# Kernel tuning notes

Hardware: AMD Instinct MI355X
Metric: run time of the kernel (lower is better)

The kernel has to match this reference:

```python
import jax, jax.numpy as jnp
import numpy as np

B, C, H, W = 32, 128, 56, 56
O = 256
KH, KW = 3, 3
SH, SW = 1, 1
PH, PW = 1, 1
T = 6          # num_terms
R = 8          # low_rank
D = C * KH * KW          # 1152
R2 = R * KH * KW         # 72


def setup_inputs() -> dict:
    key = jax.random.key(0)
    ks = jax.random.split(key, 6)
    scale = 0.05
    return {
        "x": jax.random.normal(ks[0], (B, C, H, W), dtype=jnp.float32),
        "S1s": jax.random.normal(ks[1], (T, D, R), dtype=jnp.float32) * scale,
        "U1s": jax.random.normal(ks[2], (T, R, O), dtype=jnp.float32) * scale,
        "U2s": jax.random.normal(ks[3], (T, R2, D), dtype=jnp.float32) * scale,
        "S2s": jax.random.normal(ks[4], (T, R2, O), dtype=jnp.float32) * scale,
        "bias": jax.random.normal(ks[5], (O,), dtype=jnp.float32) * scale,
    }


def _extract_windows(x):
    # im2col: pad then gather strided windows; d flattened in (C, kh, kw) order
    xp = jnp.pad(x, ((0, 0), (0, 0), (PH, PH), (PW, PW)))
    Hp, Wp = xp.shape[2], xp.shape[3]
    Ho = (Hp - KH) // SH + 1
    Wo = (Wp - KW) // SW + 1
    # stack KH*KW shifted views -> [B, C, KH*KW, Ho, Wo]
    patches = jnp.stack(
        [xp[:, :, i:i + SH * Ho:SH, j:j + SW * Wo:SW]
         for i in range(KH) for j in range(KW)],
        axis=2,
    )
    # -> [B, Ho, Wo, C, KH*KW] -> [N, C*KH*KW]
    xw = patches.transpose(0, 3, 4, 1, 2).reshape(B * Ho * Wo, D)
    return xw, Ho, Wo


def reference(x, S1s, U1s, U2s, S2s, bias):
    xw, Ho, Wo = _extract_windows(x)                    # [N, D]
    # term 1: x_windows @ S1s[t] @ U1s[t], averaged over terms
    out1 = jnp.einsum('nd,tdr,tro->no', xw, S1s, U1s, optimize=True) / T + bias
    # term 2: x_windows @ U2s[t].T @ S2s[t], averaged over terms
    out2 = jnp.einsum('nd,tdr,tro->no', xw, jnp.swapaxes(U2s, 1, 2), S2s,
                      optimize=True) / T
    # NOTE: bias is added twice, faithfully matching the original module
    out = (out1 + out2 + bias).reshape(B, Ho, Wo, O).transpose(0, 3, 1, 2)
    return out
```

## Files before the change

kernel.cpp:

```cpp
#include <hip/hip_runtime.h>
#include <hip/hip_bf16.h>

typedef __attribute__((ext_vector_type(8))) short  short8;
typedef __attribute__((ext_vector_type(8))) unsigned short ushort8;
typedef __attribute__((ext_vector_type(4))) unsigned short usv4;
typedef __attribute__((ext_vector_type(4))) float  f32x4;

#define D_DIM 1152
#define O_DIM 256
#define N_TOT 100352
#define XT_H 58
#define XT_ROW (58 * 128)

__device__ __forceinline__ unsigned short f2bf(float f) {
  __hip_bfloat16 h = __float2bfloat16(f);
  return __builtin_bit_cast(unsigned short, h);
}

#define GLOAD_LDS16(g, l)                                              \
  __builtin_amdgcn_global_load_lds(                                    \
      (const __attribute__((address_space(1))) void*)(g),              \
      (__attribute__((address_space(3))) void*)(l), 16, 0, 0)

__global__ __launch_bounds__(256) void wt_kernel(
    const float* __restrict__ S1s, const float* __restrict__ U1s,
    const float* __restrict__ U2s, const float* __restrict__ S2s,
    unsigned short* __restrict__ Wt) {
  __shared__ float A_lds[32][64];
  __shared__ float B_lds[32][64];

  const int bo = blockIdx.x & 3;
  const int bd = blockIdx.x >> 2;
  const int o0  = bo << 6;
  const int dn0 = bd << 6;
  const int rr  = dn0 >> 7;
  const int c0  = dn0 & 127;

  const int tid = threadIdx.x;
  const int ty = tid >> 4, tx = tid & 15;

  float acc[4][4] = {};

  for (int kc = 0; kc < 15; ++kc) {
#pragma unroll
    for (int e = 0; e < 8; ++e) {
      const int li = e * 256 + tid;
      const int kk = li >> 6;
      const int xx = li & 63;
      const int k  = kc * 32 + kk;
      float av, bv;
      if (k < 48) {
        av = U1s[k * O_DIM + o0 + xx];
        const int d_old = (c0 + xx) * 9 + rr;
        bv = S1s[(size_t)((k >> 3) * D_DIM + d_old) * 8 + (k & 7)];
      } else {
        const int kq = k - 48;
        av = S2s[(size_t)kq * O_DIM + o0 + xx];
        const int d_old = (c0 + xx) * 9 + rr;
        bv = U2s[(size_t)kq * D_DIM + d_old];
      }
      A_lds[kk][xx] = av;
      B_lds[kk][xx] = bv;
    }
    __syncthreads();
#pragma unroll
    for (int kk = 0; kk < 32; ++kk) {
      f32x4 a = *(const f32x4*)&A_lds[kk][ty << 2];
      f32x4 b = *(const f32x4*)&B_lds[kk][tx << 2];
#pragma unroll
      for (int i = 0; i < 4; ++i)
#pragma unroll
        for (int j = 0; j < 4; ++j)
          acc[i][j] += a[i] * b[j];
    }
    __syncthreads();
  }

#pragma unroll
  for (int i = 0; i < 4; ++i) {
    usv4 v;
#pragma unroll
    for (int j = 0; j < 4; ++j) v[j] = f2bf(acc[i][j] * (1.0f / 6.0f));
    *(usv4*)(Wt + (size_t)(o0 + (ty << 2) + i) * D_DIM + dn0 + (tx << 2)) = v;
  }
}

__global__ __launch_bounds__(256) void pad_kernel(const float* __restrict__ x,
                                                  unsigned short* __restrict__ xt) {
  int blk = blockIdx.x;
  int b = blk / XT_H, ih = blk - b * XT_H;
  unsigned short* dst = xt + (size_t)blk * XT_ROW;
  int tid = threadIdx.x;

  if (ih == 0 || ih == XT_H - 1) {
    ushort8 z;
#pragma unroll
    for (int q = 0; q < 8; ++q) z[q] = 0;
    for (int i = tid; i < XT_ROW / 8; i += 256) ((ushort8*)dst)[i] = z;
    return;
  }

  __shared__ unsigned short lds[128 * 58];
  int h = ih - 1;
  const float* xb = x + (size_t)b * 128 * 3136 + (size_t)h * 56;
#pragma unroll 4
  for (int r = 0; r < 28; ++r) {
    int idx = r * 256 + tid;
    int c = idx / 56, w2 = idx - c * 56;
    lds[c * 58 + w2] = f2bf(xb[(size_t)c * 3136 + w2]);
  }
  __syncthreads();
#pragma unroll 4
  for (int r = 0; r < 29; ++r) {
    int idx = r * 256 + tid;
    int iw = idx >> 7, c = idx & 127;
    unsigned short v = 0;
    if (iw >= 1 && iw <= 56) v = lds[c * 58 + (iw - 1)];
    dst[idx] = v;
  }
}

__device__ __forceinline__ constexpr int KOFS(int s) {
  int rr = s >> 2;
  return ((rr / 3) * 58 + (rr % 3)) * 128 + (s & 3) * 32;
}

#define STAGE_S(s_) do {                                                       \
  const int _sl = ((s_) % 3) * 12288;                                          \
  GLOAD_LDS16(pA[0] + (s_) * 32, smem + _sl + (tid << 3));                     \
  GLOAD_LDS16(pA[1] + (s_) * 32, smem + _sl + 2048 + (tid << 3));              \
  GLOAD_LDS16(pA[2] + (s_) * 32, smem + _sl + 4096 + (tid << 3));              \
  GLOAD_LDS16(pA[3] + (s_) * 32, smem + _sl + 6144 + (tid << 3));              \
  GLOAD_LDS16(pB[0] + KOFS(s_), smem + _sl + 8192 + (tid << 3));               \
  GLOAD_LDS16(pB[1] + KOFS(s_), smem + _sl + 10240 + (tid << 3));              \
} while (0)

#define AFRAG(sl_, row_)                                                       \
  (*(const short8*)((const char*)smem + (sl_) * 24576 + (row_) * 64 +        \
      (((lane >> 4) ^ (((row_) >> 1) & 3)) << 4)))
#define BFRAG(sl_, row_)                                                       \
  (*(const short8*)((const char*)smem + (sl_) * 24576 + 16384 + (row_) * 64 + \
      (((lane >> 4) ^ (((row_) >> 1) & 3)) << 4)))

__global__ __launch_bounds__(256, 2) void gemm_kernel(
    const unsigned short* __restrict__ Wt, const unsigned short* __restrict__ xt,
    const float* __restrict__ bias, float* __restrict__ out) {
  __shared__ __align__(1024) unsigned short smem[36864];

  const int bid   = blockIdx.x;
  const int ntile = (bid & 7) * 98 + (bid >> 3);
  const int n0    = ntile << 7;

  const int tid  = threadIdx.x;
  const int lane = tid & 63;
  const int w    = tid >> 6;
  const int wm   = w >> 1;
  const int wn   = w & 1;
  const int la15 = lane & 15;

  const int srow = tid >> 2;
  const int sg   = (tid & 3) ^ ((tid >> 3) & 3);
  const unsigned short* pA[4];
  const unsigned short* pB[2];
#pragma unroll
  for (int r = 0; r < 4; ++r)
    pA[r] = Wt + (size_t)(r * 64 + srow) * D_DIM + sg * 8;
#pragma unroll
  for (int r = 0; r < 2; ++r) {
    const int n_g = n0 + r * 64 + srow;
    const int b   = n_g / 3136;
    const int s   = n_g - b * 3136;
    const int oh  = s / 56, ow = s - oh * 56;
    pB[r] = xt + (((size_t)b * XT_H + oh) * XT_H + ow) * 128 + sg * 8;
  }

  f32x4 acc[8][4] = {};

  STAGE_S(0);
  STAGE_S(1);
  asm volatile("s_waitcnt vmcnt(6)" ::: "memory");
  __builtin_amdgcn_s_barrier();

#pragma unroll
  for (int s = 0; s < 36; ++s) {
    const int sl = s % 3;

    short8 afr[8], bfr[4];
#pragma unroll
    for (int mi = 0; mi < 8; ++mi)
      afr[mi] = AFRAG(sl, (wm << 7) + (mi << 4) + la15);
#pragma unroll
    for (int ni = 0; ni < 4; ++ni)
      bfr[ni] = BFRAG(sl, (wn << 6) + (ni << 4) + la15);

    if (s + 2 < 36) STAGE_S(s + 2);

    __builtin_amdgcn_s_setprio(1);
#pragma unroll
    for (int mi = 0; mi < 8; ++mi)
#pragma unroll
      for (int ni = 0; ni < 4; ++ni)
        acc[mi][ni] = __builtin_amdgcn_mfma_f32_16x16x32_bf16(
            afr[mi], bfr[ni], acc[mi][ni], 0, 0, 0);
    __builtin_amdgcn_s_setprio(0);

    if (s < 34)       asm volatile("s_waitcnt vmcnt(6)" ::: "memory");
    else if (s == 34) asm volatile("s_waitcnt vmcnt(0)" ::: "memory");
    if (s < 35) __builtin_amdgcn_s_barrier();
  }

  const int lr = (lane >> 4) << 2;
#pragma unroll
  for (int ni = 0; ni < 4; ++ni) {
    const int ng = n0 + (wn << 6) + (ni << 4) + la15;
    const int b  = ng / 3136;
    const int s  = ng - b * 3136;
    float* op = out + (size_t)b * (O_DIM * 3136) + s;
#pragma unroll
    for (int mi = 0; mi < 8; ++mi) {
      const int og = (wm << 7) + (mi << 4) + lr;
#pragma unroll
      for (int r = 0; r < 4; ++r)
        op[(size_t)(og + r) * 3136] = acc[mi][ni][r] + 2.0f * bias[og + r];
    }
  }
}

extern "C" void kernel_launch(void* const* d_in, const int* in_sizes, int n_in,
                              void* d_out, int out_size, void* d_ws, size_t ws_size,
                              hipStream_t stream) {
  const float* x    = (const float*)d_in[0];
  const float* S1s  = (const float*)d_in[1];
  const float* U1s  = (const float*)d_in[2];
  const float* U2s  = (const float*)d_in[3];
  const float* S2s  = (const float*)d_in[4];
  const float* bias = (const float*)d_in[5];
  float* out = (float*)d_out;
  (void)ws_size;

  unsigned short* xt = (unsigned short*)d_ws;
  unsigned short* Wt = (unsigned short*)((char*)d_ws + (size_t)32 * XT_H * XT_ROW * 2);

  pad_kernel<<<dim3(32 * XT_H), dim3(256), 0, stream>>>(x, xt);
  wt_kernel<<<dim3(72), dim3(256), 0, stream>>>(S1s, U1s, U2s, S2s, Wt);
  gemm_kernel<<<dim3(784), dim3(256), 0, stream>>>(Wt, xt, bias, out);
}
```

Before: 127.6 us.

## Give each wave private LDS tiles to drop block-wide barriers in GEMM

```diff
diff --git a/kernel.cpp b/kernel.cpp
--- a/kernel.cpp
+++ b/kernel.cpp
@@ -126,74 +126,76 @@
 }
 
 #define STAGE_S(s_) do {                                                       \
-  const int _sl = ((s_) % 3) * 12288;                                          \
-  GLOAD_LDS16(pA[0] + (s_) * 32, smem + _sl + (tid << 3));                     \
-  GLOAD_LDS16(pA[1] + (s_) * 32, smem + _sl + 2048 + (tid << 3));              \
-  GLOAD_LDS16(pA[2] + (s_) * 32, smem + _sl + 4096 + (tid << 3));              \
-  GLOAD_LDS16(pA[3] + (s_) * 32, smem + _sl + 6144 + (tid << 3));              \
-  GLOAD_LDS16(pB[0] + KOFS(s_), smem + _sl + 8192 + (tid << 3));               \
-  GLOAD_LDS16(pB[1] + KOFS(s_), smem + _sl + 10240 + (tid << 3));              \
+  unsigned short* _d = smem + wbe + ((s_) & 1) * 6144 + (lane << 3);           \
+  _Pragma("unroll")                                                            \
+  for (int c = 0; c < 8; ++c)                                                  \
+    GLOAD_LDS16(pA[c] + (s_) * 32, _d + c * 512);                              \
+  _Pragma("unroll")                                                            \
+  for (int c = 0; c < 4; ++c)                                                  \
+    GLOAD_LDS16(pB[c] + KOFS(s_), _d + 4096 + c * 512);                        \
 } while (0)
 
-#define AFRAG(sl_, row_)                                                       \
-  (*(const short8*)((const char*)smem + (sl_) * 24576 + (row_) * 64 +        \
+#define AFRAG(q_, row_)                                                        \
+  (*(const short8*)((const char*)smem + wbb + (q_) * 12288 + (row_) * 64 +    \
       (((lane >> 4) ^ (((row_) >> 1) & 3)) << 4)))
-#define BFRAG(sl_, row_)                                                       \
-  (*(const short8*)((const char*)smem + (sl_) * 24576 + 16384 + (row_) * 64 + \
-      (((lane >> 4) ^ (((row_) >> 1) & 3)) << 4)))
-
-__global__ __launch_bounds__(256, 2) void gemm_kernel(
+#define BFRAG(q_, row_)                                                        \
+  (*(const short8*)((const char*)smem + wbb + (q_) * 12288 + 8192 +           \
+      (row_) * 64 + (((lane >> 4) ^ (((row_) >> 1) & 3)) << 4)))
+
+__global__ __launch_bounds__(256, 1) void gemm_kernel(
     const unsigned short* __restrict__ Wt, const unsigned short* __restrict__ xt,
     const float* __restrict__ bias, float* __restrict__ out) {
-  __shared__ __align__(1024) unsigned short smem[36864];
+  __shared__ __align__(1024) unsigned short smem[49152];
 
   const int bid   = blockIdx.x;
-  const int ntile = (bid & 7) * 98 + (bid >> 3);
-  const int n0    = ntile << 7;
+  const int lid   = (bid & 7) * 98 + (bid >> 3);
+  const int ntile = lid >> 1;
+  const int ohalf = lid & 1;
+  const int obase = ohalf << 7;
 
   const int tid  = threadIdx.x;
   const int lane = tid & 63;
   const int w    = tid >> 6;
-  const int wm   = w >> 1;
-  const int wn   = w & 1;
+  const int n_w  = (ntile << 8) + (w << 6);
   const int la15 = lane & 15;
 
-  const int srow = tid >> 2;
-  const int sg   = (tid & 3) ^ ((tid >> 3) & 3);
-  const unsigned short* pA[4];
-  const unsigned short* pB[2];
-#pragma unroll
-  for (int r = 0; r < 4; ++r)
-    pA[r] = Wt + (size_t)(r * 64 + srow) * D_DIM + sg * 8;
-#pragma unroll
-  for (int r = 0; r < 2; ++r) {
-    const int n_g = n0 + r * 64 + srow;
+  const int wbe = w * 12288;
+  const int wbb = w * 24576;
+
+  const int srow = lane >> 2;
+  const int sg   = (lane & 3) ^ ((lane >> 3) & 3);
+  const unsigned short* pA[8];
+  const unsigned short* pB[4];
+#pragma unroll
+  for (int c = 0; c < 8; ++c)
+    pA[c] = Wt + (size_t)(obase + c * 16 + srow) * D_DIM + sg * 8;
+#pragma unroll
+  for (int c = 0; c < 4; ++c) {
+    const int n_g = n_w + c * 16 + srow;
     const int b   = n_g / 3136;
     const int s   = n_g - b * 3136;
     const int oh  = s / 56, ow = s - oh * 56;
-    pB[r] = xt + (((size_t)b * XT_H + oh) * XT_H + ow) * 128 + sg * 8;
+    pB[c] = xt + (((size_t)b * XT_H + oh) * XT_H + ow) * 128 + sg * 8;
   }
 
   f32x4 acc[8][4] = {};
 
   STAGE_S(0);
-  STAGE_S(1);
-  asm volatile("s_waitcnt vmcnt(6)" ::: "memory");
-  __builtin_amdgcn_s_barrier();
+  asm volatile("s_waitcnt vmcnt(0)" ::: "memory");
 
 #pragma unroll
   for (int s = 0; s < 36; ++s) {
-    const int sl = s % 3;
+    const int q = s & 1;
+
+    if (s + 1 < 36) STAGE_S(s + 1);
 
     short8 afr[8], bfr[4];
 #pragma unroll
     for (int mi = 0; mi < 8; ++mi)
-      afr[mi] = AFRAG(sl, (wm << 7) + (mi << 4) + la15);
+      afr[mi] = AFRAG(q, mi * 16 + la15);
 #pragma unroll
     for (int ni = 0; ni < 4; ++ni)
-      bfr[ni] = BFRAG(sl, (wn << 6) + (ni << 4) + la15);
-
-    if (s + 2 < 36) STAGE_S(s + 2);
+      bfr[ni] = BFRAG(q, ni * 16 + la15);
 
     __builtin_amdgcn_s_setprio(1);
 #pragma unroll
@@ -204,21 +206,19 @@
             afr[mi], bfr[ni], acc[mi][ni], 0, 0, 0);
     __builtin_amdgcn_s_setprio(0);
 
-    if (s < 34)       asm volatile("s_waitcnt vmcnt(6)" ::: "memory");
-    else if (s == 34) asm volatile("s_waitcnt vmcnt(0)" ::: "memory");
-    if (s < 35) __builtin_amdgcn_s_barrier();
+    if (s + 1 < 36) asm volatile("s_waitcnt vmcnt(0)" ::: "memory");
   }
 
   const int lr = (lane >> 4) << 2;
 #pragma unroll
   for (int ni = 0; ni < 4; ++ni) {
-    const int ng = n0 + (wn << 6) + (ni << 4) + la15;
+    const int ng = n_w + ni * 16 + la15;
     const int b  = ng / 3136;
     const int s  = ng - b * 3136;
     float* op = out + (size_t)b * (O_DIM * 3136) + s;
 #pragma unroll
     for (int mi = 0; mi < 8; ++mi) {
-      const int og = (wm << 7) + (mi << 4) + lr;
+      const int og = obase + mi * 16 + lr;
 #pragma unroll
       for (int r = 0; r < 4; ++r)
         op[(size_t)(og + r) * 3136] = acc[mi][ni][r] + 2.0f * bias[og + r];
```

Measured after the change: 142.3 us. 1.11x slower.

## Enlarge GEMM tile to 256x256 with 8 waves, 4-stage LDS ring and fragment prefetch

Applied to the files above, without the earlier changes.

```diff
diff --git a/kernel.cpp b/kernel.cpp
--- a/kernel.cpp
+++ b/kernel.cpp
@@ -126,48 +126,53 @@
 }
 
 #define STAGE_S(s_) do {                                                       \
-  const int _sl = ((s_) % 3) * 12288;                                          \
-  GLOAD_LDS16(pA[0] + (s_) * 32, smem + _sl + (tid << 3));                     \
-  GLOAD_LDS16(pA[1] + (s_) * 32, smem + _sl + 2048 + (tid << 3));              \
-  GLOAD_LDS16(pA[2] + (s_) * 32, smem + _sl + 4096 + (tid << 3));              \
-  GLOAD_LDS16(pA[3] + (s_) * 32, smem + _sl + 6144 + (tid << 3));              \
-  GLOAD_LDS16(pB[0] + KOFS(s_), smem + _sl + 8192 + (tid << 3));               \
-  GLOAD_LDS16(pB[1] + KOFS(s_), smem + _sl + 10240 + (tid << 3));              \
+  unsigned short* _d = smem + ((s_) & 3) * 16384 + (tid << 3);                 \
+  GLOAD_LDS16(pA[0] + (s_) * 32, _d);                                          \
+  GLOAD_LDS16(pA[1] + (s_) * 32, _d + 4096);                                   \
+  GLOAD_LDS16(pB[0] + KOFS(s_), _d + 8192);                                    \
+  GLOAD_LDS16(pB[1] + KOFS(s_), _d + 12288);                                   \
 } while (0)
 
 #define AFRAG(sl_, row_)                                                       \
-  (*(const short8*)((const char*)smem + (sl_) * 24576 + (row_) * 64 +        \
+  (*(const short8*)((const char*)smem + (sl_) * 32768 + (row_) * 64 +        \
       (((lane >> 4) ^ (((row_) >> 1) & 3)) << 4)))
 #define BFRAG(sl_, row_)                                                       \
-  (*(const short8*)((const char*)smem + (sl_) * 24576 + 16384 + (row_) * 64 + \
+  (*(const short8*)((const char*)smem + (sl_) * 32768 + 16384 + (row_) * 64 + \
       (((lane >> 4) ^ (((row_) >> 1) & 3)) << 4)))
 
-__global__ __launch_bounds__(256, 2) void gemm_kernel(
+#define READ_FRAGS(set_, sl_) do {                                             \
+  _Pragma("unroll")                                                            \
+  for (int mi = 0; mi < 8; ++mi)                                               \
+    fA[set_][mi] = AFRAG(sl_, (wm << 7) + (mi << 4) + la15);                   \
+  _Pragma("unroll")                                                            \
+  for (int ni = 0; ni < 4; ++ni)                                               \
+    fB[set_][ni] = BFRAG(sl_, (wn << 6) + (ni << 4) + la15);                   \
+} while (0)
+
+__global__ __launch_bounds__(512, 1) void gemm_kernel(
     const unsigned short* __restrict__ Wt, const unsigned short* __restrict__ xt,
     const float* __restrict__ bias, float* __restrict__ out) {
-  __shared__ __align__(1024) unsigned short smem[36864];
+  __shared__ __align__(1024) unsigned short smem[65536];
 
   const int bid   = blockIdx.x;
-  const int ntile = (bid & 7) * 98 + (bid >> 3);
-  const int n0    = ntile << 7;
+  const int ntile = (bid & 7) * 49 + (bid >> 3);
+  const int n0    = ntile << 8;
 
   const int tid  = threadIdx.x;
   const int lane = tid & 63;
   const int w    = tid >> 6;
-  const int wm   = w >> 1;
-  const int wn   = w & 1;
+  const int wm   = w >> 2;
+  const int wn   = w & 3;
   const int la15 = lane & 15;
 
   const int srow = tid >> 2;
   const int sg   = (tid & 3) ^ ((tid >> 3) & 3);
-  const unsigned short* pA[4];
+  const unsigned short* pA[2];
   const unsigned short* pB[2];
 #pragma unroll
-  for (int r = 0; r < 4; ++r)
-    pA[r] = Wt + (size_t)(r * 64 + srow) * D_DIM + sg * 8;
-#pragma unroll
   for (int r = 0; r < 2; ++r) {
-    const int n_g = n0 + r * 64 + srow;
+    pA[r] = Wt + (size_t)(r * 128 + srow) * D_DIM + sg * 8;
+    const int n_g = n0 + r * 128 + srow;
     const int b   = n_g / 3136;
     const int s   = n_g - b * 3136;
     const int oh  = s / 56, ow = s - oh * 56;
@@ -175,25 +180,27 @@
   }
 
   f32x4 acc[8][4] = {};
+  short8 fA[2][8], fB[2][4];
 
   STAGE_S(0);
   STAGE_S(1);
-  asm volatile("s_waitcnt vmcnt(6)" ::: "memory");
+  STAGE_S(2);
+  asm volatile("s_waitcnt vmcnt(8)" ::: "memory");
   __builtin_amdgcn_s_barrier();
-
-#pragma unroll
-  for (int s = 0; s < 36; ++s) {
-    const int sl = s % 3;
-
-    short8 afr[8], bfr[4];
-#pragma unroll
-    for (int mi = 0; mi < 8; ++mi)
-      afr[mi] = AFRAG(sl, (wm << 7) + (mi << 4) + la15);
-#pragma unroll
-    for (int ni = 0; ni < 4; ++ni)
-      bfr[ni] = BFRAG(sl, (wn << 6) + (ni << 4) + la15);
-
-    if (s + 2 < 36) STAGE_S(s + 2);
+  READ_FRAGS(0, 0);
+
+#pragma unroll
+  for (int j = 0; j < 36; ++j) {
+    const int cur = j & 1;
+    const int nxt = cur ^ 1;
+
+    if (j + 3 < 36) STAGE_S(j + 3);
+
+    if (j <= 32)      asm volatile("s_waitcnt vmcnt(4)" ::: "memory");
+    else if (j == 33) asm volatile("s_waitcnt vmcnt(4)" ::: "memory");
+    else if (j == 34) asm volatile("s_waitcnt vmcnt(0)" ::: "memory");
+
+    if (j + 1 < 36) READ_FRAGS(nxt, (j + 1) & 3);
 
     __builtin_amdgcn_s_setprio(1);
 #pragma unroll
@@ -201,12 +208,10 @@
 #pragma unroll
       for (int ni = 0; ni < 4; ++ni)
         acc[mi][ni] = __builtin_amdgcn_mfma_f32_16x16x32_bf16(
-            afr[mi], bfr[ni], acc[mi][ni], 0, 0, 0);
+            fA[cur][mi], fB[cur][ni], acc[mi][ni], 0, 0, 0);
     __builtin_amdgcn_s_setprio(0);
 
-    if (s < 34)       asm volatile("s_waitcnt vmcnt(6)" ::: "memory");
-    else if (s == 34) asm volatile("s_waitcnt vmcnt(0)" ::: "memory");
-    if (s < 35) __builtin_amdgcn_s_barrier();
+    if (j + 1 < 36) __builtin_amdgcn_s_barrier();
   }
 
   const int lr = (lane >> 4) << 2;
@@ -243,5 +248,5 @@
 
   pad_kernel<<<dim3(32 * XT_H), dim3(256), 0, stream>>>(x, xt);
   wt_kernel<<<dim3(72), dim3(256), 0, stream>>>(S1s, U1s, U2s, S2s, Wt);
-  gemm_kernel<<<dim3(784), dim3(256), 0, stream>>>(Wt, xt, bias, out);
-}
+  gemm_kernel<<<dim3(392), dim3(512), 0, stream>>>(Wt, xt, bias, out);
+}
```

Result: faster. 124.1 us (-2.8%).
